# Kernel optimization log

Measured on AMD Instinct MI355X. Metric: run time of the kernel, lower is better.

The kernel has to match this reference:

```python
import jax, jax.numpy as jnp
import numpy as np
from jax import lax

B, SEQ, C, H, W, OUT, K = 64, 32, 16, 128, 256, 10, 2  # batch, timestamps, channels, hidden, width, classes, substeps/interval


def setup_inputs() -> dict:
    key = jax.random.key(0)
    ks = jax.random.split(key, 16)
    p = lambda k, shape, fan_in: (jax.random.normal(k, shape, dtype=jnp.float32) / np.sqrt(fan_in))
    coeff = lambda k: jax.random.normal(k, (B, SEQ - 1, C), dtype=jnp.float32)
    return {
        'ts': jnp.arange(SEQ, dtype=jnp.float32),
        'coeff_d': coeff(ks[0]), 'coeff_c': coeff(ks[1]), 'coeff_b': coeff(ks[2]), 'coeff_a': coeff(ks[3]),
        # initial MLP: in_size -> width -> width -> hidden (relu)
        'iw0': p(ks[4], (W, C), C), 'ib0': jnp.zeros((W,), jnp.float32),
        'iw1': p(ks[5], (W, W), W), 'ib1': jnp.zeros((W,), jnp.float32),
        'iw2': p(ks[6], (H, W), W), 'ib2': jnp.zeros((H,), jnp.float32),
        # vector-field MLP: hidden -> width -> width -> hidden*in_size (softplus, tanh final)
        'fw0': p(ks[7], (W, H), H), 'fb0': jnp.zeros((W,), jnp.float32),
        'fw1': p(ks[8], (W, W), W), 'fb1': jnp.zeros((W,), jnp.float32),
        'fw2': p(ks[9], (H * C, W), W), 'fb2': jnp.zeros((H * C,), jnp.float32),
        # readout linear: hidden -> out
        'lw': p(ks[10], (OUT, H), H), 'lb': jnp.zeros((OUT,), jnp.float32),
    }


def _forward(ts, coeff_d, coeff_c, coeff_b, coeff_a, iw0, ib0, iw1, ib1, iw2, ib2,
             fw0, fb0, fw1, fb1, fw2, fb2, lw, lb):
    nb, ni, c = coeff_a.shape
    h_dim = iw2.shape[0]

    def init_mlp(x):  # [B,C] -> [B,H]
        h = jax.nn.relu(x @ iw0.T + ib0)
        h = jax.nn.relu(h @ iw1.T + ib1)
        return h @ iw2.T + ib2

    def vf(y):  # [B,H] -> [B,H,C]
        h = jax.nn.softplus(y @ fw0.T + fb0)
        h = jax.nn.softplus(h @ fw1.T + fb1)
        return jnp.tanh(h @ fw2.T + fb2).reshape(nb, h_dim, c)

    def dxdt(frac, i):  # derivative of cubic interpolation on interval i: 3d f^2 + 2c f + b
        return (3.0 * coeff_d[:, i] * frac + 2.0 * coeff_c[:, i]) * frac + coeff_b[:, i]

    def f(frac, i, y):  # ControlTerm.to_ode: dy/dt = vf(y) @ dX/dt
        return jnp.einsum('bhc,bc->bh', vf(y), dxdt(frac, i))

    dts = jnp.diff(ts)
    hsub = dts / K
    idx = jnp.repeat(jnp.arange(ni), K)                                # interval index per substep
    hs = jnp.repeat(hsub, K)                                           # substep size
    fr0 = jnp.tile(jnp.arange(K, dtype=ts.dtype), ni) * hs             # offset within interval at substep start

    def step(y, xs):  # one fixed-size Tsit5 step (Tsitouras 2011 tableau)
        t0, h, i = xs
        k1 = f(t0, i, y)
        k2 = f(t0 + 0.161 * h, i, y + h * (0.161 * k1))
        k3 = f(t0 + 0.327 * h, i, y + h * (-0.008480655492356989 * k1 + 0.335480655492357 * k2))
        k4 = f(t0 + 0.9 * h, i, y + h * (2.8971530571054935 * k1 - 6.359448489975075 * k2 + 4.3622954328695815 * k3))
        k5 = f(t0 + 0.9800255409045097 * h, i, y + h * (5.325864828439257 * k1 - 11.748883564062828 * k2 + 7.4955393428898365 * k3 - 0.09249506636175525 * k4))
        k6 = f(t0 + h, i, y + h * (5.86145544294642 * k1 - 12.92096931784711 * k2 + 8.159367898576159 * k3 - 0.071584973281401 * k4 - 0.028269050394068383 * k5))
        y_new = y + h * (0.09646076681806523 * k1 + 0.01 * k2 + 0.4798896504144996 * k3 + 1.379008574103742 * k4 - 3.290069515436081 * k5 + 2.324710524099774 * k6)
        return y_new, None

    y0 = init_mlp(coeff_a[:, 0])  # X(ts[0]) = a-coefficient at frac=0
    yT, _ = lax.scan(step, y0, (fr0, hs, idx))
    return jax.nn.log_softmax(yT @ lw.T + lb, axis=-1)  # out_size != 1 -> log_softmax


def reference(ts, coeff_d, coeff_c, coeff_b, coeff_a, iw0, ib0, iw1, ib1, iw2, ib2,
              fw0, fb0, fw1, fb1, fw2, fb2, lw, lb):
    return _forward(ts, coeff_d, coeff_c, coeff_b, coeff_a, iw0, ib0, iw1, ib1, iw2, ib2,
                    fw0, fb0, fw1, fb1, fw2, fb2, lw, lb)
```

## Files before the change

### kernel.cpp

```cpp
#include <hip/hip_runtime.h>

#define NBATCH 64
#define NSEQ   32
#define NI     31
#define NC     16
#define NH     128
#define NW     256
#define NOUT   10
#define NSUB   62

#define NGRP 8
#define GB   8
#define NSL  32
#define NBLK (NGRP*NSL)
#define BS   512

#define L1R 8
#define L2R 8
#define L3H 4
#define L3R 64

#define P128 132
#define P256 260

#define WS_BAR   0
#define WS_H1    4096
#define WS_H2    (4096 + 65536)
#define WS_KV    (4096 + 131072)

__device__ const float ATAB[6][5] = {
  {0.f, 0.f, 0.f, 0.f, 0.f},
  {0.161f, 0.f, 0.f, 0.f, 0.f},
  {-0.008480655492356989f, 0.335480655492357f, 0.f, 0.f, 0.f},
  {2.8971530571054935f, -6.359448489975075f, 4.3622954328695815f, 0.f, 0.f},
  {5.325864828439257f, -11.748883564062828f, 7.4955393428898365f, -0.09249506636175525f, 0.f},
  {5.86145544294642f, -12.92096931784711f, 8.159367898576159f, -0.071584973281401f, -0.028269050394068383f}
};
__device__ const float CNODE[6] = {0.f, 0.161f, 0.327f, 0.9f, 0.9800255409045097f, 1.f};
__device__ const float BTAB[6]  = {0.09646076681806523f, 0.01f, 0.4798896504144996f,
                                   1.379008574103742f, -3.290069515436081f, 2.324710524099774f};

__device__ __forceinline__ float softplusf_(float x) {
  return fmaxf(x, 0.0f) + log1pf(expf(-fabsf(x)));
}
__device__ __forceinline__ float dot4(float4 a, float4 b) {
  return (a.x*b.x + a.y*b.y) + (a.z*b.z + a.w*b.w);
}

__device__ __forceinline__ void gstore(float* p, float v) {
  __hip_atomic_store(p, v, __ATOMIC_RELAXED, __HIP_MEMORY_SCOPE_AGENT);
}
__device__ __forceinline__ float gload(const float* p) {
  return __hip_atomic_load(p, __ATOMIC_RELAXED, __HIP_MEMORY_SCOPE_AGENT);
}

__device__ __forceinline__ void group_barrier(unsigned* cnt, unsigned target) {
  __syncthreads();
  if (threadIdx.x == 0) {
    __hip_atomic_fetch_add(cnt, 1u, __ATOMIC_RELAXED, __HIP_MEMORY_SCOPE_AGENT);
    while (__hip_atomic_load(cnt, __ATOMIC_RELAXED, __HIP_MEMORY_SCOPE_AGENT) < target) {
      __builtin_amdgcn_s_sleep(1);
    }
  }
  __syncthreads();
}

__global__ void bar_init(unsigned* bar) {
  if (threadIdx.x < NGRP * 16) bar[threadIdx.x] = 0u;
}

__global__ __launch_bounds__(BS) void ncde_fwd(
    const float* __restrict__ ts,
    const float* __restrict__ cd, const float* __restrict__ cc,
    const float* __restrict__ cb, const float* __restrict__ ca,
    const float* __restrict__ iw0, const float* __restrict__ ib0,
    const float* __restrict__ iw1, const float* __restrict__ ib1,
    const float* __restrict__ iw2, const float* __restrict__ ib2,
    const float* __restrict__ fw0, const float* __restrict__ fb0,
    const float* __restrict__ fw1, const float* __restrict__ fb1,
    const float* __restrict__ fw2, const float* __restrict__ fb2,
    const float* __restrict__ lw,  const float* __restrict__ lb,
    unsigned* __restrict__ bar, float* __restrict__ h1g, float* __restrict__ h2g,
    float* __restrict__ kvg, float* __restrict__ out)
{
  const int t   = threadIdx.x;
  const int g   = blockIdx.x & 7;
  const int s   = blockIdx.x >> 3;
  const int gr0 = g * GB;
  unsigned* bcnt = bar + g * 16;
  unsigned  btarget = 0;

  __shared__ float fw0s[L1R][P128];
  __shared__ float fw1s[L2R][P256];
  __shared__ float fw2s[L3R][P256];
  __shared__ float h1s[GB][P256];
  __shared__ float h2s[GB][P256];
  __shared__ float ysv[GB][P128];
  __shared__ float yloc[GB][NH];
  __shared__ float dxs[GB][NC];
  __shared__ float x0s[GB][NC];
  __shared__ float fb0s[L1R], fb1s[L2R], fb2s[L3R];
  __shared__ float tss[NSEQ];
  __shared__ float lgs[GB][NOUT], lses[GB];

  {
    if (t < 256) {
      int row = t >> 5, j = t & 31;
      *(float4*)&fw0s[row][4*j] = *(const float4*)&fw0[(size_t)(s*L1R + row)*NH + 4*j];
    }
    {
      int r2 = t >> 6, j2 = t & 63;
      *(float4*)&fw1s[r2][4*j2] = *(const float4*)&fw1[(size_t)(s*L2R + r2)*NW + 4*j2];
    }
    #pragma unroll
    for (int i = 0; i < 8; ++i) {
      int e = t + BS*i; int r2 = e >> 6, j2 = e & 63;
      *(float4*)&fw2s[r2][4*j2] = *(const float4*)&fw2[(size_t)(s*L3R + r2)*NW + 4*j2];
    }
    if (t < L1R) fb0s[t] = fb0[s*L1R + t];
    if (t < L2R) fb1s[t] = fb1[s*L2R + t];
    if (t < L3R) fb2s[t] = fb2[s*L3R + t];
    if (t < NSEQ) tss[t] = ts[t];
  }

  if (t < GB*NC) { int r = t >> 4, c = t & 15; x0s[r][c] = ca[((size_t)(gr0 + r)*NI)*NC + c]; }
  __syncthreads();
  #pragma unroll
  for (int i = 0; i < 4; ++i) {
    int e = t + BS*i; int r = e >> 8, row = e & 255;
    float a = ib0[row];
    #pragma unroll
    for (int k = 0; k < NC; ++k) a += iw0[row*NC + k] * x0s[r][k];
    h1s[r][row] = fmaxf(a, 0.f);
  }
  __syncthreads();
  #pragma unroll
  for (int i = 0; i < 4; ++i) {
    int e = t + BS*i; int r = e >> 8, row = e & 255;
    float a = ib1[row];
    const float4* wr = (const float4*)&iw1[(size_t)row*NW];
    for (int k = 0; k < 64; ++k) a += dot4(wr[k], *(const float4*)&h1s[r][4*k]);
    h2s[r][row] = fmaxf(a, 0.f);
  }
  __syncthreads();
  #pragma unroll
  for (int i = 0; i < 2; ++i) {
    int e = t + BS*i; int r = e >> 7, row = e & 127;
    float a = ib2[row];
    const float4* wr = (const float4*)&iw2[(size_t)row*NW];
    for (int k = 0; k < 64; ++k) a += dot4(wr[k], *(const float4*)&h2s[r][4*k]);
    yloc[r][row] = a;
  }
  __syncthreads();

  const int yr  = t >> 5, yc4 = 4*(t & 31);
  const int o   = t >> 3, q8 = t & 7;
  const int orow = o & 7, obat = o >> 3;
  const int l3row = t & 63, l3h = l3row >> 4, l3c = l3row & 15, l3b = t >> 6;

  for (int ss = 0; ss < NSUB; ++ss) {
    const int iv = ss >> 1, jv = ss & 1;
    const float h = (tss[iv+1] - tss[iv]) * 0.5f;
    const float t0f = (float)jv * h;

    float cdv = 0.f, ccv = 0.f, cbv = 0.f;
    if (t >= 256 && t < 256 + GB*NC) {
      const int tc = t - 256;
      const size_t base = ((size_t)(gr0 + (tc >> 4))*NI + iv)*NC + (tc & 15);
      cdv = cd[base]; ccv = cc[base]; cbv = cb[base];
    }

    for (int st = 0; st < 6; ++st) {
      if (t < 256) {
        float4 v = *(const float4*)&yloc[yr][yc4];
        for (int jj = 0; jj < st; ++jj) {
          const float* kp = &kvg[((size_t)jj*NBATCH + gr0 + yr)*NH + yc4];
          const float a = h * ATAB[st][jj];
          v.x += a*gload(kp+0); v.y += a*gload(kp+1);
          v.z += a*gload(kp+2); v.w += a*gload(kp+3);
        }
        *(float4*)&ysv[yr][yc4] = v;
      } else if (t < 256 + GB*NC) {
        const int tc = t - 256;
        const float f = t0f + CNODE[st] * h;
        dxs[tc >> 4][tc & 15] = (3.f*cdv*f + 2.f*ccv)*f + cbv;
      }
      __syncthreads();

      {
        float a0 = 0.f, a1 = 0.f;
        #pragma unroll
        for (int i = 0; i < 4; i += 2) {
          a0 += dot4(*(const float4*)&fw0s[orow][4*(q8+8*i)],     *(const float4*)&ysv[obat][4*(q8+8*i)]);
          a1 += dot4(*(const float4*)&fw0s[orow][4*(q8+8*(i+1))], *(const float4*)&ysv[obat][4*(q8+8*(i+1))]);
        }
        float a = a0 + a1;
        a += __shfl_xor(a, 1); a += __shfl_xor(a, 2); a += __shfl_xor(a, 4);
        if (q8 == 0) gstore(&h1g[(gr0 + obat)*NW + s*L1R + orow], softplusf_(fb0s[orow] + a));
      }
      group_barrier(bcnt, btarget += NSL);

      #pragma unroll
      for (int i = 0; i < 4; ++i) {
        int e = t + BS*i; int r = e >> 8, col = e & 255;
        h1s[r][col] = gload(&h1g[(gr0 + r)*NW + col]);
      }
      __syncthreads();

      {
        float a0 = 0.f, a1 = 0.f;
        #pragma unroll
        for (int i = 0; i < 8; i += 2) {
          a0 += dot4(*(const float4*)&fw1s[orow][4*(q8+8*i)],     *(const float4*)&h1s[obat][4*(q8+8*i)]);
          a1 += dot4(*(const float4*)&fw1s[orow][4*(q8+8*(i+1))], *(const float4*)&h1s[obat][4*(q8+8*(i+1))]);
        }
        float a = a0 + a1;
        a += __shfl_xor(a, 1); a += __shfl_xor(a, 2); a += __shfl_xor(a, 4);
        if (q8 == 0) gstore(&h2g[(gr0 + obat)*NW + s*L2R + orow], softplusf_(fb1s[orow] + a));
      }
      group_barrier(bcnt, btarget += NSL);

      #pragma unroll
      for (int i = 0; i < 4; ++i) {
        int e = t + BS*i; int r = e >> 8, col = e & 255;
        h2s[r][col] = gload(&h2g[(gr0 + r)*NW + col]);
      }
      __syncthreads();

      {
        const float4* wr = (const float4*)&fw2s[l3row][0];
        const float4* xr = (const float4*)&h2s[l3b][0];
        float a0 = 0.f, a1 = 0.f, a2 = 0.f, a3 = 0.f;
        #pragma unroll 4
        for (int i = 0; i < 64; i += 4) {
          a0 += dot4(wr[i+0], xr[i+0]);
          a1 += dot4(wr[i+1], xr[i+1]);
          a2 += dot4(wr[i+2], xr[i+2]);
          a3 += dot4(wr[i+3], xr[i+3]);
        }
        float v0 = tanhf(((a0+a1)+(a2+a3)) + fb2s[l3row]) * dxs[l3b][l3c];
        v0 += __shfl_xor(v0, 1);
        v0 += __shfl_xor(v0, 2);
        v0 += __shfl_xor(v0, 4);
        v0 += __shfl_xor(v0, 8);
        if (l3c == 0) gstore(&kvg[((size_t)st*NBATCH + gr0 + l3b)*NH + s*L3H + l3h], v0);
      }
      group_barrier(bcnt, btarget += NSL);
    }

    if (t < 256) {
      float4 v = *(const float4*)&yloc[yr][yc4];
      #pragma unroll
      for (int s2 = 0; s2 < 6; ++s2) {
        const float* kp = &kvg[((size_t)s2*NBATCH + gr0 + yr)*NH + yc4];
        const float a = h * BTAB[s2];
        v.x += a*gload(kp+0); v.y += a*gload(kp+1);
        v.z += a*gload(kp+2); v.w += a*gload(kp+3);
      }
      *(float4*)&yloc[yr][yc4] = v;
    }
    __syncthreads();
  }

  if (s == 0) {
    if (t < GB*NOUT) {
      const int r = t / NOUT, oo = t % NOUT;
      float a = lb[oo];
      const float4* wr = (const float4*)&lw[(size_t)oo*NH];
      #pragma unroll
      for (int k = 0; k < 32; ++k) a += dot4(wr[k], *(const float4*)&yloc[r][4*k]);
      lgs[r][oo] = a;
    }
    __syncthreads();
    if (t < GB) {
      float m = lgs[t][0];
      for (int oo = 1; oo < NOUT; ++oo) m = fmaxf(m, lgs[t][oo]);
      float se = 0.f;
      for (int oo = 0; oo < NOUT; ++oo) se += expf(lgs[t][oo] - m);
      lses[t] = m + logf(se);
    }
    __syncthreads();
    if (t < GB*NOUT) {
      const int r = t / NOUT, oo = t % NOUT;
      out[(gr0 + r)*NOUT + oo] = lgs[r][oo] - lses[r];
    }
  }
}

extern "C" void kernel_launch(void* const* d_in, const int* in_sizes, int n_in,
                              void* d_out, int out_size, void* d_ws, size_t ws_size,
                              hipStream_t stream) {
  const float* ts  = (const float*)d_in[0];
  const float* cd  = (const float*)d_in[1];
  const float* cc  = (const float*)d_in[2];
  const float* cb  = (const float*)d_in[3];
  const float* ca  = (const float*)d_in[4];
  const float* iw0 = (const float*)d_in[5];
  const float* ib0 = (const float*)d_in[6];
  const float* iw1 = (const float*)d_in[7];
  const float* ib1 = (const float*)d_in[8];
  const float* iw2 = (const float*)d_in[9];
  const float* ib2 = (const float*)d_in[10];
  const float* fw0 = (const float*)d_in[11];
  const float* fb0 = (const float*)d_in[12];
  const float* fw1 = (const float*)d_in[13];
  const float* fb1 = (const float*)d_in[14];
  const float* fw2 = (const float*)d_in[15];
  const float* fb2 = (const float*)d_in[16];
  const float* lw  = (const float*)d_in[17];
  const float* lb  = (const float*)d_in[18];

  char* ws = (char*)d_ws;
  unsigned* bar = (unsigned*)(ws + WS_BAR);
  float* h1g = (float*)(ws + WS_H1);
  float* h2g = (float*)(ws + WS_H2);
  float* kvg = (float*)(ws + WS_KV);

  bar_init<<<1, 128, 0, stream>>>(bar);
  ncde_fwd<<<NBLK, BS, 0, stream>>>(ts, cd, cc, cb, ca, iw0, ib0, iw1, ib1, iw2, ib2,
                                    fw0, fb0, fw1, fb1, fw2, fb2, lw, lb,
                                    bar, h1g, h2g, kvg, (float*)d_out);
}
```

Baseline: 4.361 ms.

## Replace atomic-counter group barrier with per-block flag slots and cache RK stages in registers

The group barrier changes from one shared atomic counter that every block increments to per-block sequence slots, each padded to its own cache line. Each block publishes its sequence number, and one wavefront polls all 32 slots and uses a wave vote to decide when to proceed, removing contention on a single atomic. The RK stage vectors and the state y are now kept in registers: each stage result is loaded once after its barrier, instead of re-reading every earlier stage from global memory in later stages and in the final combination. This costs more registers (kreg holds 6 float4 values) and more polling traffic, since 64 threads per block each load a slot.

```diff
diff --git a/kernel.cpp b/kernel.cpp
--- a/kernel.cpp
+++ b/kernel.cpp
@@ -24,9 +24,9 @@
 #define P256 260
 
 #define WS_BAR   0
-#define WS_H1    4096
-#define WS_H2    (4096 + 65536)
-#define WS_KV    (4096 + 131072)
+#define WS_H1    16384
+#define WS_H2    (16384 + 65536)
+#define WS_KV    (16384 + 131072)
 
 __device__ const float ATAB[6][5] = {
   {0.f, 0.f, 0.f, 0.f, 0.f},
@@ -54,19 +54,29 @@
   return __hip_atomic_load(p, __ATOMIC_RELAXED, __HIP_MEMORY_SCOPE_AGENT);
 }
 
-__device__ __forceinline__ void group_barrier(unsigned* cnt, unsigned target) {
+#define SLOT_STRIDE 16
+__device__ __forceinline__ void group_barrier(unsigned* slots, int myslot, unsigned seq) {
   __syncthreads();
   if (threadIdx.x == 0) {
-    __hip_atomic_fetch_add(cnt, 1u, __ATOMIC_RELAXED, __HIP_MEMORY_SCOPE_AGENT);
-    while (__hip_atomic_load(cnt, __ATOMIC_RELAXED, __HIP_MEMORY_SCOPE_AGENT) < target) {
-      __builtin_amdgcn_s_sleep(1);
+    __hip_atomic_store(&slots[myslot * SLOT_STRIDE], seq,
+                       __ATOMIC_RELAXED, __HIP_MEMORY_SCOPE_AGENT);
+  }
+  if (threadIdx.x < 64) {
+    const int lane = threadIdx.x & 31;
+    for (;;) {
+      const unsigned v = __hip_atomic_load(&slots[lane * SLOT_STRIDE],
+                                           __ATOMIC_RELAXED, __HIP_MEMORY_SCOPE_AGENT);
+      if (__all(v >= seq)) break;
+      __builtin_amdgcn_s_sleep(2);
     }
   }
   __syncthreads();
 }
 
 __global__ void bar_init(unsigned* bar) {
-  if (threadIdx.x < NGRP * 16) bar[threadIdx.x] = 0u;
+  const int n = NGRP * NSL * SLOT_STRIDE;
+  for (int i = threadIdx.x; i < n; i += blockDim.x)
+    __hip_atomic_store(&bar[i], 0u, __ATOMIC_RELAXED, __HIP_MEMORY_SCOPE_AGENT);
 }
 
 __global__ __launch_bounds__(BS) void ncde_fwd(
@@ -87,8 +97,8 @@
   const int g   = blockIdx.x & 7;
   const int s   = blockIdx.x >> 3;
   const int gr0 = g * GB;
-  unsigned* bcnt = bar + g * 16;
-  unsigned  btarget = 0;
+  unsigned* slots = bar + g * NSL * SLOT_STRIDE;
+  unsigned  bseq  = 0;
 
   __shared__ float fw0s[L1R][P128];
   __shared__ float fw1s[L2R][P256];
@@ -158,6 +168,9 @@
   const int orow = o & 7, obat = o >> 3;
   const int l3row = t & 63, l3h = l3row >> 4, l3c = l3row & 15, l3b = t >> 6;
 
+  float4 yreg, kreg[6];
+  if (t < 256) yreg = *(const float4*)&yloc[yr][yc4];
+
   for (int ss = 0; ss < NSUB; ++ss) {
     const int iv = ss >> 1, jv = ss & 1;
     const float h = (tss[iv+1] - tss[iv]) * 0.5f;
@@ -172,12 +185,11 @@
 
     for (int st = 0; st < 6; ++st) {
       if (t < 256) {
-        float4 v = *(const float4*)&yloc[yr][yc4];
+        float4 v = yreg;
         for (int jj = 0; jj < st; ++jj) {
-          const float* kp = &kvg[((size_t)jj*NBATCH + gr0 + yr)*NH + yc4];
           const float a = h * ATAB[st][jj];
-          v.x += a*gload(kp+0); v.y += a*gload(kp+1);
-          v.z += a*gload(kp+2); v.w += a*gload(kp+3);
+          v.x += a*kreg[jj].x; v.y += a*kreg[jj].y;
+          v.z += a*kreg[jj].z; v.w += a*kreg[jj].w;
         }
         *(float4*)&ysv[yr][yc4] = v;
       } else if (t < 256 + GB*NC) {
@@ -198,7 +210,7 @@
         a += __shfl_xor(a, 1); a += __shfl_xor(a, 2); a += __shfl_xor(a, 4);
         if (q8 == 0) gstore(&h1g[(gr0 + obat)*NW + s*L1R + orow], softplusf_(fb0s[orow] + a));
       }
-      group_barrier(bcnt, btarget += NSL);
+      group_barrier(slots, s, ++bseq);
 
       #pragma unroll
       for (int i = 0; i < 4; ++i) {
@@ -218,7 +230,7 @@
         a += __shfl_xor(a, 1); a += __shfl_xor(a, 2); a += __shfl_xor(a, 4);
         if (q8 == 0) gstore(&h2g[(gr0 + obat)*NW + s*L2R + orow], softplusf_(fb1s[orow] + a));
       }
-      group_barrier(bcnt, btarget += NSL);
+      group_barrier(slots, s, ++bseq);
 
       #pragma unroll
       for (int i = 0; i < 4; ++i) {
@@ -245,22 +257,27 @@
         v0 += __shfl_xor(v0, 8);
         if (l3c == 0) gstore(&kvg[((size_t)st*NBATCH + gr0 + l3b)*NH + s*L3H + l3h], v0);
       }
-      group_barrier(bcnt, btarget += NSL);
+      group_barrier(slots, s, ++bseq);
+
+      if (t < 256) {
+        const float* kp = &kvg[((size_t)st*NBATCH + gr0 + yr)*NH + yc4];
+        kreg[st].x = gload(kp+0); kreg[st].y = gload(kp+1);
+        kreg[st].z = gload(kp+2); kreg[st].w = gload(kp+3);
+      }
     }
 
     if (t < 256) {
-      float4 v = *(const float4*)&yloc[yr][yc4];
       #pragma unroll
       for (int s2 = 0; s2 < 6; ++s2) {
-        const float* kp = &kvg[((size_t)s2*NBATCH + gr0 + yr)*NH + yc4];
         const float a = h * BTAB[s2];
-        v.x += a*gload(kp+0); v.y += a*gload(kp+1);
-        v.z += a*gload(kp+2); v.w += a*gload(kp+3);
-      }
-      *(float4*)&yloc[yr][yc4] = v;
-    }
-    __syncthreads();
-  }
+        yreg.x += a*kreg[s2].x; yreg.y += a*kreg[s2].y;
+        yreg.z += a*kreg[s2].z; yreg.w += a*kreg[s2].w;
+      }
+    }
+  }
+
+  if (t < 256) *(float4*)&yloc[yr][yc4] = yreg;
+  __syncthreads();
 
   if (s == 0) {
     if (t < GB*NOUT) {
@@ -316,7 +333,7 @@
   float* h2g = (float*)(ws + WS_H2);
   float* kvg = (float*)(ws + WS_KV);
 
-  bar_init<<<1, 128, 0, stream>>>(bar);
+  bar_init<<<1, 512, 0, stream>>>(bar);
   ncde_fwd<<<NBLK, BS, 0, stream>>>(ts, cd, cc, cb, ca, iw0, ib0, iw1, ib1, iw2, ib2,
                                     fw0, fb0, fw1, fb1, fw2, fb2, lw, lb,
                                     bar, h1g, h2g, kvg, (float*)d_out);
```

Measured after the change: 4.136 ms. 1.05x faster.
